# Kernel tuning notes

Measured on AMD Instinct MI355X. Metric: run time of the kernel, lower is better.

## Reference

```python
import jax, jax.numpy as jnp
import numpy as np

BS, NQ, DIMS = 4, 6400, 256
NH, NL, NP, NQUEUE = 8, 1, 4, 2


def ms_deform_attn(value, shapes_np, starts_np, loc, attn):
    # value: [B, Nv, H, D]; loc: [B, Nq, H, L, P, 2] in [0,1]; attn: [B, Nq, H, L, P]
    B, Nv, H, D = value.shape
    _, Nq, _, L, P, _ = loc.shape
    out = jnp.zeros((B, H, Nq, D), loc.dtype)
    for l in range(L):
        Hl, Wl = int(shapes_np[l, 0]), int(shapes_np[l, 1])
        s = int(starts_np[l])
        vl = value[:, s:s + Hl * Wl].transpose(0, 2, 1, 3)  # [B,H,HW,D]
        # grid_sample align_corners=False pixel coords
        x = loc[:, :, :, l, :, 0] * Wl - 0.5  # [B,Nq,H,P]
        y = loc[:, :, :, l, :, 1] * Hl - 0.5
        x0 = jnp.floor(x); y0 = jnp.floor(y)
        dx = x - x0; dy = y - y0
        x0i = x0.astype(jnp.int32); y0i = y0.astype(jnp.int32)
        acc = jnp.zeros((B, H, Nq * P, D), loc.dtype)
        corners = [(x0i, y0i, (1 - dx) * (1 - dy)),
                   (x0i + 1, y0i, dx * (1 - dy)),
                   (x0i, y0i + 1, (1 - dx) * dy),
                   (x0i + 1, y0i + 1, dx * dy)]
        for xi, yi, w in corners:
            valid = (xi >= 0) & (xi < Wl) & (yi >= 0) & (yi < Hl)
            idx = jnp.clip(yi, 0, Hl - 1) * Wl + jnp.clip(xi, 0, Wl - 1)  # [B,Nq,H,P]
            idx_t = idx.transpose(0, 2, 1, 3).reshape(B, H, Nq * P, 1)
            g = jnp.take_along_axis(vl, idx_t, axis=2)  # [B,H,Nq*P,D]
            wv = jnp.where(valid, w, 0.0).transpose(0, 2, 1, 3).reshape(B, H, Nq * P, 1)
            acc = acc + g * wv
        acc = acc.reshape(B, H, Nq, P, D)
        wl = attn[:, :, :, l].transpose(0, 2, 1, 3)  # [B,H,Nq,P]
        out = out + jnp.einsum('bhnpd,bhnp->bhnd', acc, wl)
    return out.transpose(0, 2, 1, 3).reshape(B, Nq, H * D)


def setup_inputs() -> dict:
    key = jax.random.key(0)
    ks = jax.random.split(key, 12)
    d2 = DIMS * NQUEUE
    noff = NQUEUE * NH * NL * NP * 2
    nattn = NQUEUE * NH * NL * NP
    sc = 1.0 / np.sqrt(DIMS)
    return {
        'query': jax.random.normal(ks[0], (BS, NQ, DIMS), jnp.float32),
        'voxbev': jax.random.normal(ks[1], (BS, NQ, DIMS), jnp.float32),
        'reference_points': jax.random.uniform(ks[2], (BS * NQUEUE, NQ, NL, 2), jnp.float32),
        'spatial_shapes': jnp.array([[80, 80]], dtype=jnp.int64),
        'level_start_index': jnp.array([0], dtype=jnp.int64),
        'Wv': jax.random.normal(ks[3], (DIMS, DIMS), jnp.float32) * sc,
        'bv': jax.random.normal(ks[4], (DIMS,), jnp.float32) * 0.01,
        'Woff': jax.random.normal(ks[5], (d2, noff), jnp.float32) * (1.0 / np.sqrt(d2)),
        'boff': jax.random.normal(ks[6], (noff,), jnp.float32),
        'Wattn': jax.random.normal(ks[7], (d2, nattn), jnp.float32) * (1.0 / np.sqrt(d2)),
        'battn': jax.random.normal(ks[8], (nattn,), jnp.float32) * 0.01,
        'Wo': jax.random.normal(ks[9], (DIMS, DIMS), jnp.float32) * sc,
        'bo': jax.random.normal(ks[10], (DIMS,), jnp.float32) * 0.01,
    }


def reference(query, voxbev, reference_points, spatial_shapes, level_start_index,
              Wv, bv, Woff, boff, Wattn, battn, Wo, bo):
    bs, nq, dims = query.shape
    shapes_np = np.asarray(spatial_shapes)
    starts_np = np.asarray(level_start_index)
    identity = query
    # value = stack([query, voxbev], 1).reshape(bs*2, nq, dims) -> interleaved [q0,v0,q1,v1,...]
    value = jnp.stack([query, voxbev], 1).reshape(bs * NQUEUE, nq, dims)
    qcat = jnp.concatenate([value[:bs], query], -1)  # [bs, nq, 2*dims]
    v = (value @ Wv + bv).reshape(bs * NQUEUE, nq, NH, dims // NH)
    off = (qcat @ Woff + boff).reshape(bs, nq, NH, NQUEUE, NL, NP, 2)
    attn = (qcat @ Wattn + battn).reshape(bs, nq, NH, NQUEUE, NL * NP)
    attn = jax.nn.softmax(attn, axis=-1).reshape(bs, nq, NH, NQUEUE, NL, NP)
    attn = attn.transpose(0, 3, 1, 2, 4, 5).reshape(bs * NQUEUE, nq, NH, NL, NP)
    off = off.transpose(0, 3, 1, 2, 4, 5, 6).reshape(bs * NQUEUE, nq, NH, NL, NP, 2)
    # offset normalizer: (W, H) per level
    norm = jnp.stack([spatial_shapes[:, 1], spatial_shapes[:, 0]], -1).astype(off.dtype)  # [L,2]
    loc = reference_points[:, :, None, :, None, :] + off / norm[None, None, None, :, None, :]
    out = ms_deform_attn(v, shapes_np, starts_np, loc, attn)  # [bs*2, nq, dims]
    out = out.reshape(bs, NQUEUE, nq, dims).mean(1)  # mean over queue
    out = out @ Wo + bo
    return out + identity  # dropout is identity in eval
```

## Files before the change

kernel.cpp:

```cpp
#include <hip/hip_runtime.h>
#include <hip/hip_bf16.h>

#define BS   4
#define NQ   6400
#define DIMS 256
#define NH   8
#define NP   4
#define GW   80
#define GH   80

typedef __hip_bfloat16 bf16;
typedef unsigned short ushort;
typedef __attribute__((ext_vector_type(8))) short short8;
typedef __attribute__((ext_vector_type(4))) float floatx4;

union bfu { bf16 h; ushort s; };
__device__ __forceinline__ ushort f2bs(float x) { bfu u; u.h = __float2bfloat16(x); return u.s; }
__device__ __forceinline__ float bs2f(ushort s) { return __uint_as_float(((unsigned)s) << 16); }
__device__ __forceinline__ float ldin(const void* p, size_t i, int isf) {
    return isf ? ((const float*)p)[i] : bs2f(((const ushort*)p)[i]);
}

__device__ __forceinline__ void gl_lds16(const void* gsrc, void* ldst) {
    __builtin_amdgcn_global_load_lds(
        (const __attribute__((address_space(1))) unsigned int*)gsrc,
        (__attribute__((address_space(3))) unsigned int*)ldst,
        16, 0, 0);
}

__device__ __forceinline__ int self_detect(const ushort* __restrict__ q, int tid) {
    int bad = 0;
    const uint4 u0 = ((const uint4*)q)[tid * 2];
    const uint4 u1 = ((const uint4*)q)[tid * 2 + 1];
    const unsigned w[8] = { u0.x, u0.y, u0.z, u0.w, u1.x, u1.y, u1.z, u1.w };
    #pragma unroll
    for (int j = 0; j < 8; ++j) {
        if (((w[j] >> 7)  & 0xFF) > 160) bad = 1;
        if (((w[j] >> 23) & 0xFF) > 160) bad = 1;
    }
    return __any(bad) ? 1 : 0;
}

__global__ __launch_bounds__(256) void prep_k(
    const void* __restrict__ Wv, const void* __restrict__ bv,
    const void* __restrict__ Woff, const void* __restrict__ boff,
    const void* __restrict__ Wattn, const void* __restrict__ battn,
    const void* __restrict__ Wo, const void* __restrict__ bo,
    int* __restrict__ flagp,
    ushort* __restrict__ WvT, ushort* __restrict__ WoaT, ushort* __restrict__ WoT,
    float* __restrict__ biasv, float* __restrict__ biasoa, float* __restrict__ biaso,
    const void* __restrict__ query, const void* __restrict__ voxbev,
    uint4* __restrict__ qb, uint4* __restrict__ vbv)
{
    const int tid = threadIdx.x;
    const int isf = self_detect((const ushort*)query, tid);
    const int bid = blockIdx.x;
    if (bid == 0 && tid == 0) *flagp = isf;
    if (bid < 899) {
        const int i = bid * 256 + tid;
        const int n1 = 256 * 256, n2 = n1 + 192 * 512, n3 = n2 + 256 * 256;
        const int n4 = n3 + 256, n5 = n4 + 192, n6 = n5 + 256;
        if (i < n1) {
            int n = i >> 8, k = i & 255;
            WvT[i] = f2bs(ldin(Wv, (size_t)k * 256 + n, isf));
        } else if (i < n2) {
            int j = i - n1, n = j >> 9, k = j & 511;
            float v = (n < 128) ? ldin(Woff, (size_t)k * 128 + n, isf)
                                : ldin(Wattn, (size_t)k * 64 + (n - 128), isf);
            WoaT[j] = f2bs(v);
        } else if (i < n3) {
            int j = i - n2, n = j >> 8, k = j & 255;
            WoT[j] = f2bs(ldin(Wo, (size_t)k * 256 + n, isf));
        } else if (i < n4) {
            biasv[i - n3] = ldin(bv, i - n3, isf);
        } else if (i < n5) {
            int j = i - n4;
            biasoa[j] = (j < 128) ? ldin(boff, j, isf) : ldin(battn, j - 128, isf);
        } else if (i < n6) {
            biaso[i - n5] = ldin(bo, i - n5, isf);
        }
    } else {
        if (isf == 0) return;
        const int t = (bid - 899) * 256 + tid;
        const int half = 819200;
        const void* src = (t < half) ? query : voxbev;
        uint4* dst = (t < half) ? qb : vbv;
        const int j = (t < half) ? t : t - half;
        const float4* s = (const float4*)src + (size_t)j * 2;
        float4 a = s[0], b = s[1];
        uint4 o;
        o.x = ((unsigned)f2bs(a.y) << 16) | f2bs(a.x);
        o.y = ((unsigned)f2bs(a.w) << 16) | f2bs(a.z);
        o.z = ((unsigned)f2bs(b.y) << 16) | f2bs(b.x);
        o.w = ((unsigned)f2bs(b.w) << 16) | f2bs(b.z);
        dst[j] = o;
    }
}

enum { A_VAL = 0, A_QCAT = 1, A_PLAIN = 2 };
enum { O_BF16 = 0, O_FINAL = 1, O_VPERM = 2, O_OAPERM = 3 };

#define ABYT 16384
#define BBYT 8192
#define CST  67
#define SMEMB (ABYT + BBYT)

template <int AMODE, int OMODE, int KTOT, int NX, int MG>
__device__ __forceinline__ void pgemm_body(
    const int F, char* smem,
    const ushort* __restrict__ Apl, const ushort* __restrict__ BT,
    const float* __restrict__ biasf, void* __restrict__ C,
    const void* __restrict__ query_raw, const void* __restrict__ voxbev_raw,
    const ushort* __restrict__ qb, const ushort* __restrict__ vbv,
    const int isf)
{
    constexpr int N = NX * 64;
    constexpr int NT = KTOT / 64;
    float* cbf = (float*)smem;

    const int xcd = F & 7, l = F >> 3;
    const int n = l % NX;
    const int mg = (l / NX) * 8 + xcd;
    if (mg >= MG) return;
    const int bm = mg * 128, bn = n * 64;

    const int tid = threadIdx.x;
    const int lane = tid & 63, wv = tid >> 6;
    const int wm = wv * 32;
    const int fr = lane & 15;
    const int lrow = lane >> 3;
    const int lslot = lane & 7;
    const int sg = lslot ^ lrow;

    const ushort* qsrc = isf ? qb  : (const ushort*)query_raw;
    const ushort* vsrc = isf ? vbv : (const ushort*)voxbev_raw;
    const ushort* aph[2] = { nullptr, nullptr };
    if (AMODE == A_PLAIN) {
        aph[0] = Apl + (size_t)bm * DIMS;
    } else {
        const int b = bm / NQ, q0 = bm - (bm / NQ) * NQ;
        aph[0] = ((b & 1) ? vsrc : qsrc) + (size_t)((b >> 1) * NQ + q0) * DIMS;
        if (AMODE == A_QCAT) aph[1] = qsrc + (size_t)(b * NQ + q0) * DIMS;
    }

    floatx4 acc[2][4] = {};

    #pragma unroll
    for (int t = 0; t < NT; ++t) {
        if (t > 0) __syncthreads();
        #pragma unroll
        for (int c4 = 0; c4 < 4; ++c4) {
            const int c = wv * 4 + c4;
            const int row = c * 8 + lrow;
            const int k = t * 64 + sg * 8;
            const ushort* gp;
            if (AMODE == A_QCAT && KTOT == 512)
                gp = aph[k >> 8] + (size_t)row * DIMS + (k & 255);
            else
                gp = aph[0] + (size_t)row * DIMS + k;
            gl_lds16(gp, smem + c * 1024);
        }
        #pragma unroll
        for (int c2 = 0; c2 < 2; ++c2) {
            const int c = wv * 2 + c2;
            const int row = c * 8 + lrow;
            gl_lds16(&BT[(size_t)(bn + row) * KTOT + t * 64 + sg * 8],
                     smem + ABYT + c * 1024);
        }
        asm volatile("s_waitcnt vmcnt(0)" ::: "memory");
        __syncthreads();

        const short* acur = (const short*)smem;
        const short* bcur = (const short*)(smem + ABYT);
        #pragma unroll
        for (int k0 = 0; k0 < 64; k0 += 32) {
            const int gl = (k0 >> 3) + (lane >> 4);
            const int sl = gl ^ (fr & 7);
            short8 af[2], bf[4];
            #pragma unroll
            for (int mt = 0; mt < 2; ++mt)
                af[mt] = *(const short8*)&acur[(wm + mt * 16 + fr) * 64 + sl * 8];
            #pragma unroll
            for (int nt = 0; nt < 4; ++nt)
                bf[nt] = *(const short8*)&bcur[(nt * 16 + fr) * 64 + sl * 8];
            #pragma unroll
            for (int mt = 0; mt < 2; ++mt)
                #pragma unroll
                for (int nt = 0; nt < 4; ++nt)
                    acc[mt][nt] = __builtin_amdgcn_mfma_f32_16x16x32_bf16(
                        af[mt], bf[nt], acc[mt][nt], 0, 0, 0);
        }
    }

    const int col = lane & 15, rq = (lane >> 4) * 4;
    const int lbase = wm & 63;
    #pragma unroll
    for (int half = 0; half < 2; ++half) {
        __syncthreads();
        if ((wv >> 1) == half) {
            #pragma unroll
            for (int mt = 0; mt < 2; ++mt)
                #pragma unroll
                for (int nt = 0; nt < 4; ++nt)
                    #pragma unroll
                    for (int r = 0; r < 4; ++r)
                        cbf[(lbase + mt * 16 + rq + r) * CST + nt * 16 + col] =
                            acc[mt][nt][r];
        }
        __syncthreads();

        if (OMODE == O_FINAL && isf) {
            const int r16 = tid >> 4, cc = tid & 15;
            #pragma unroll
            for (int it = 0; it < 4; ++it) {
                const int lr = it * 16 + r16;
                const size_t g = (size_t)(bm + half * 64 + lr);
                float4 x = *(const float4*)&cbf[lr * CST + cc * 4];
                const ushort* rs = qsrc + g * DIMS + bn + cc * 4;
                x.x += biasf[bn + cc * 4 + 0] + bs2f(rs[0]);
                x.y += biasf[bn + cc * 4 + 1] + bs2f(rs[1]);
                x.z += biasf[bn + cc * 4 + 2] + bs2f(rs[2]);
                x.w += biasf[bn + cc * 4 + 3] + bs2f(rs[3]);
                *(float4*)((float*)C + g * N + bn + cc * 4) = x;
            }
        } else {
            const int r8 = tid >> 3, c8 = tid & 7;
            #pragma unroll
            for (int it = 0; it < 2; ++it) {
                const int lr = it * 32 + r8;
                const size_t g = (size_t)(bm + half * 64 + lr);
                float4 x0 = *(const float4*)&cbf[lr * CST + c8 * 8];
                float4 x1 = *(const float4*)&cbf[lr * CST + c8 * 8 + 4];
                float xs[8] = { x0.x, x0.y, x0.z, x0.w, x1.x, x1.y, x1.z, x1.w };
                #pragma unroll
                for (int e = 0; e < 8; ++e) xs[e] += biasf[bn + c8 * 8 + e];
                if (OMODE == O_FINAL) {
                    const ushort* rs = qsrc + g * DIMS + bn + c8 * 8;
                    #pragma unroll
                    for (int e = 0; e < 8; ++e) xs[e] += bs2f(rs[e]);
                }
                uint4 o;
                o.x = ((unsigned)f2bs(xs[1]) << 16) | f2bs(xs[0]);
                o.y = ((unsigned)f2bs(xs[3]) << 16) | f2bs(xs[2]);
                o.z = ((unsigned)f2bs(xs[5]) << 16) | f2bs(xs[4]);
                o.w = ((unsigned)f2bs(xs[7]) << 16) | f2bs(xs[6]);
                ushort* dstp;
                if (OMODE == O_VPERM) {
                    const int cc = bn + c8 * 8;
                    const int s = (int)(g / NQ), qq = (int)(g % NQ);
                    dstp = (ushort*)C + ((size_t)(s * 8 + (cc >> 5)) * NQ + qq) * 32
                                      + (cc & 31);
                } else if (OMODE == O_OAPERM) {
                    const int cc = bn + c8 * 8;
                    const int bb = (int)(g / NQ), qq = (int)(g % NQ);
                    int hh, off;
                    if (cc < 128) { hh = cc >> 4; off = cc & 15; }
                    else          { hh = (cc - 128) >> 3; off = 16; }
                    dstp = (ushort*)C + ((size_t)(bb * 8 + hh) * NQ + qq) * 24 + off;
                } else {
                    dstp = (ushort*)C + g * N + bn + c8 * 8;
                }
                *(uint4*)dstp = o;
            }
        }
    }
}

__global__ __launch_bounds__(256, 6) void gemm12_k(
    const ushort* __restrict__ WvT, const float* __restrict__ biasv,
    ushort* __restrict__ v_ws,
    const ushort* __restrict__ WoaT, const float* __restrict__ biasoa,
    ushort* __restrict__ offraw,
    const void* __restrict__ query_raw, const void* __restrict__ voxbev_raw,
    const ushort* __restrict__ qb, const ushort* __restrict__ vbv,
    const int* __restrict__ flagp)
{
    __shared__ __align__(16) char smem[SMEMB];
    const int isf = *flagp;
    const int bid = blockIdx.x;
    if (bid < 1600) {
        pgemm_body<A_VAL, O_VPERM, 256, 4, 400>(bid, smem,
            nullptr, WvT, biasv, (void*)v_ws, query_raw, voxbev_raw, qb, vbv, isf);
    } else {
        pgemm_body<A_QCAT, O_OAPERM, 512, 3, 200>(bid - 1600, smem,
            nullptr, WoaT, biasoa, (void*)offraw, query_raw, voxbev_raw, qb, vbv, isf);
    }
}

__global__ __launch_bounds__(256, 6) void gemm4_k(
    const ushort* __restrict__ Apl, const ushort* __restrict__ BT,
    const float* __restrict__ biasf, void* __restrict__ C,
    const void* __restrict__ query_raw, const void* __restrict__ voxbev_raw,
    const ushort* __restrict__ qb, const ushort* __restrict__ vbv,
    const int* __restrict__ flagp)
{
    __shared__ __align__(16) char smem[SMEMB];
    const int isf = *flagp;
    pgemm_body<A_PLAIN, O_FINAL, 256, 4, 200>(blockIdx.x, smem,
        Apl, BT, biasf, C, query_raw, voxbev_raw, qb, vbv, isf);
}

__global__ __launch_bounds__(256) void sample_k(
    const ushort* __restrict__ v,
    const ushort* __restrict__ offp,
    const void* __restrict__ refpts,
    const int* __restrict__ flagp,
    ushort* __restrict__ sampled)
{
    const int isf = *flagp;
    __shared__ int   sidx[64][2][17];
    __shared__ float swt [64][2][17];
    const int tid = threadIdx.x;
    const int j = blockIdx.x;
    const int h = j & 7;
    const int k = j >> 3;
    const int b = k / 100;
    const int q0 = (k % 100) * 64;

    if (tid < 128) {
        const int lq = tid >> 1, queue = tid & 1;
        const int q = q0 + lq;
        const ushort* rec = offp + ((size_t)(b * 8 + h) * NQ + q) * 24;
        const ushort* al = rec + 16 + queue * 4;
        float l0 = bs2f(al[0]), l1 = bs2f(al[1]), l2 = bs2f(al[2]), l3 = bs2f(al[3]);
        float mx = fmaxf(fmaxf(l0, l1), fmaxf(l2, l3));
        float e0 = __expf(l0 - mx), e1 = __expf(l1 - mx);
        float e2 = __expf(l2 - mx), e3 = __expf(l3 - mx);
        float inv = 0.5f / (e0 + e1 + e2 + e3);
        const int bq = b * 2 + queue;
        const float rx = ldin(refpts, ((size_t)bq * NQ + q) * 2 + 0, isf);
        const float ry = ldin(refpts, ((size_t)bq * NQ + q) * 2 + 1, isf);
        const ushort* od = rec + queue * 8;
        float ww[4] = { e0 * inv, e1 * inv, e2 * inv, e3 * inv };
        #pragma unroll
        for (int p = 0; p < NP; ++p) {
            const float x = rx * (float)GW + bs2f(od[p * 2 + 0]) - 0.5f;
            const float y = ry * (float)GH + bs2f(od[p * 2 + 1]) - 0.5f;
            const float x0f = floorf(x), y0f = floorf(y);
            const float dx = x - x0f, dy = y - y0f;
            const int x0 = (int)x0f, y0 = (int)y0f;
            const float wp = ww[p];
            const float cw4[4] = { wp * (1.0f - dx) * (1.0f - dy),
                                   wp * dx * (1.0f - dy),
                                   wp * (1.0f - dx) * dy,
                                   wp * dx * dy };
            #pragma unroll
            for (int c = 0; c < 4; ++c) {
                const int xs = x0 + (c & 1), ys = y0 + (c >> 1);
                const bool ok = (unsigned)xs < (unsigned)GW && (unsigned)ys < (unsigned)GH;
                const int xi = min(max(xs, 0), GW - 1);
                const int yi = min(max(ys, 0), GH - 1);
                sidx[lq][queue][p * 4 + c] = yi * GW + xi;
                swt [lq][queue][p * 4 + c] = ok ? cw4[c] : 0.0f;
            }
        }
    }
    __syncthreads();

    const int lq = tid >> 2, d8 = tid & 3;
    const int q = q0 + lq;
    float a[8] = {};
    #pragma unroll
    for (int queue = 0; queue < 2; ++queue) {
        const ushort* vb = v + (((size_t)(b * 2 + queue) * 8 + h) * NQ) * 32 + d8 * 8;
        #pragma unroll
        for (int hf = 0; hf < 2; ++hf) {
            uint4 g[8];
            #pragma unroll
            for (int u = 0; u < 8; ++u) {
                const int ci = sidx[lq][queue][hf * 8 + u];
                g[u] = *(const uint4*)&vb[(size_t)ci * 32];
            }
            __builtin_amdgcn_sched_barrier(0);
            #pragma unroll
            for (int u = 0; u < 8; ++u) {
                const float cw = swt[lq][queue][hf * 8 + u];
                a[0] += cw * bs2f((ushort)g[u].x); a[1] += cw * bs2f((ushort)(g[u].x >> 16));
                a[2] += cw * bs2f((ushort)g[u].y); a[3] += cw * bs2f((ushort)(g[u].y >> 16));
                a[4] += cw * bs2f((ushort)g[u].z); a[5] += cw * bs2f((ushort)(g[u].z >> 16));
                a[6] += cw * bs2f((ushort)g[u].w); a[7] += cw * bs2f((ushort)(g[u].w >> 16));
            }
        }
    }
    uint4 o;
    o.x = ((unsigned)f2bs(a[1]) << 16) | f2bs(a[0]);
    o.y = ((unsigned)f2bs(a[3]) << 16) | f2bs(a[2]);
    o.z = ((unsigned)f2bs(a[5]) << 16) | f2bs(a[4]);
    o.w = ((unsigned)f2bs(a[7]) << 16) | f2bs(a[6]);
    *(uint4*)&sampled[((size_t)b * NQ + q) * DIMS + h * 32 + d8 * 8] = o;
}

extern "C" void kernel_launch(void* const* d_in, const int* in_sizes, int n_in,
                              void* d_out, int out_size, void* d_ws, size_t ws_size,
                              hipStream_t stream)
{
    const void* query  = d_in[0];
    const void* voxbev = d_in[1];
    const void* refpts = d_in[2];
    const void* Wv   = d_in[5];  const void* bv    = d_in[6];
    const void* Woff = d_in[7];  const void* boff  = d_in[8];
    const void* Wattn= d_in[9];  const void* battn = d_in[10];
    const void* Wo   = d_in[11]; const void* bo    = d_in[12];

    char* p = (char*)d_ws;
    int* flag = (int*)p;             p += 256;
    ushort* WvT  = (ushort*)p;       p += 256 * 256 * 2;
    ushort* WoaT = (ushort*)p;       p += 192 * 512 * 2;
    ushort* WoT  = (ushort*)p;       p += 256 * 256 * 2;
    float* biasv  = (float*)p;       p += 1024;
    float* biasoa = (float*)p;       p += 1024;
    float* biaso  = (float*)p;       p += 1024;
    ushort* qb   = (ushort*)p;       p += (size_t)BS * NQ * DIMS * 2;
    ushort* vbv  = (ushort*)p;       p += (size_t)BS * NQ * DIMS * 2;
    ushort* v_ws = (ushort*)p;       p += (size_t)2 * BS * NQ * DIMS * 2;
    ushort* offraw = (ushort*)p;     p += (size_t)BS * NQ * 192 * 2;
    ushort* sampled = (ushort*)p;

    prep_k<<<7299, 256, 0, stream>>>(Wv, bv, Woff, boff, Wattn, battn, Wo, bo,
                                     flag, WvT, WoaT, WoT, biasv, biasoa, biaso,
                                     query, voxbev, (uint4*)qb, (uint4*)vbv);

    gemm12_k<<<2200, 256, 0, stream>>>(WvT, biasv, v_ws, WoaT, biasoa, offraw,
                                       query, voxbev, qb, vbv, flag);

    sample_k<<<3200, 256, 0, stream>>>(v_ws, offraw, refpts, flag, sampled);

    gemm4_k<<<800, 256, 0, stream>>>(sampled, WoT, biaso, d_out,
                                     query, voxbev, qb, vbv, flag);
}
```

Baseline: 190.6 us.

## Fuse all stages into one cooperative persistent kernel with double-buffered GEMM loads

Replaces the four separate launches with a single cooperative kernel of 768 persistent blocks that loop over the work of each stage, separated by grid-wide syncs. This removes launch gaps and the inter-kernel drain. The GEMM body now double-buffers its LDS tiles so the next K-tile's global-to-LDS loads overlap the current MFMAs, and the epilogue writes the full 128-row tile in one pass instead of two halves. The flag buffer is dropped and each block recomputes the dtype detection itself. The costs are larger shared memory, which limits occupancy to 3 blocks per CU, grid-sync overhead, and a fallback to separate launches if the cooperative launch fails.

```diff
diff --git a/kernel.cpp b/kernel.cpp
--- a/kernel.cpp
+++ b/kernel.cpp
@@ -1,5 +1,8 @@
 #include <hip/hip_runtime.h>
 #include <hip/hip_bf16.h>
+#include <hip/hip_cooperative_groups.h>
+
+namespace cg = cooperative_groups;
 
 #define BS   4
 #define NQ   6400
@@ -26,6 +29,12 @@
         (const __attribute__((address_space(1))) unsigned int*)gsrc,
         (__attribute__((address_space(3))) unsigned int*)ldst,
         16, 0, 0);
+}
+
+__device__ __forceinline__ void barrier_fence() {
+    __builtin_amdgcn_sched_barrier(0);
+    asm volatile("s_barrier" ::: "memory");
+    __builtin_amdgcn_sched_barrier(0);
 }
 
 __device__ __forceinline__ int self_detect(const ushort* __restrict__ q, int tid) {
@@ -41,23 +50,19 @@
     return __any(bad) ? 1 : 0;
 }
 
-__global__ __launch_bounds__(256) void prep_k(
+__device__ __forceinline__ void prep_body(
+    const int vb, const int tid, const int isf,
     const void* __restrict__ Wv, const void* __restrict__ bv,
     const void* __restrict__ Woff, const void* __restrict__ boff,
     const void* __restrict__ Wattn, const void* __restrict__ battn,
     const void* __restrict__ Wo, const void* __restrict__ bo,
-    int* __restrict__ flagp,
     ushort* __restrict__ WvT, ushort* __restrict__ WoaT, ushort* __restrict__ WoT,
     float* __restrict__ biasv, float* __restrict__ biasoa, float* __restrict__ biaso,
     const void* __restrict__ query, const void* __restrict__ voxbev,
     uint4* __restrict__ qb, uint4* __restrict__ vbv)
 {
-    const int tid = threadIdx.x;
-    const int isf = self_detect((const ushort*)query, tid);
-    const int bid = blockIdx.x;
-    if (bid == 0 && tid == 0) *flagp = isf;
-    if (bid < 899) {
-        const int i = bid * 256 + tid;
+    if (vb < 899) {
+        const int i = vb * 256 + tid;
         const int n1 = 256 * 256, n2 = n1 + 192 * 512, n3 = n2 + 256 * 256;
         const int n4 = n3 + 256, n5 = n4 + 192, n6 = n5 + 256;
         if (i < n1) {
@@ -81,7 +86,7 @@
         }
     } else {
         if (isf == 0) return;
-        const int t = (bid - 899) * 256 + tid;
+        const int t = (vb - 899) * 256 + tid;
         const int half = 819200;
         const void* src = (t < half) ? query : voxbev;
         uint4* dst = (t < half) ? qb : vbv;
@@ -100,13 +105,11 @@
 enum { A_VAL = 0, A_QCAT = 1, A_PLAIN = 2 };
 enum { O_BF16 = 0, O_FINAL = 1, O_VPERM = 2, O_OAPERM = 3 };
 
-#define ABYT 16384
-#define BBYT 8192
-#define CST  67
-#define SMEMB (ABYT + BBYT)
-
-template <int AMODE, int OMODE, int KTOT, int NX, int MG>
-__device__ __forceinline__ void pgemm_body(
+#define PTILE 24576
+#define PSMEM (2 * PTILE)
+
+template <int AMODE, int OMODE, int KTOT, int NXW, int MG>
+__device__ __forceinline__ void pgemm_pipe(
     const int F, char* smem,
     const ushort* __restrict__ Apl, const ushort* __restrict__ BT,
     const float* __restrict__ biasf, void* __restrict__ C,
@@ -114,13 +117,13 @@
     const ushort* __restrict__ qb, const ushort* __restrict__ vbv,
     const int isf)
 {
-    constexpr int N = NX * 64;
+    constexpr int N = 64 * NXW;
     constexpr int NT = KTOT / 64;
     float* cbf = (float*)smem;
 
     const int xcd = F & 7, l = F >> 3;
-    const int n = l % NX;
-    const int mg = (l / NX) * 8 + xcd;
+    const int n = l % NXW;
+    const int mg = (l / NXW) * 8 + xcd;
     if (mg >= MG) return;
     const int bm = mg * 128, bn = n * 64;
 
@@ -143,11 +146,9 @@
         if (AMODE == A_QCAT) aph[1] = qsrc + (size_t)(b * NQ + q0) * DIMS;
     }
 
-    floatx4 acc[2][4] = {};
-
-    #pragma unroll
-    for (int t = 0; t < NT; ++t) {
-        if (t > 0) __syncthreads();
+    auto stage = [&](int td, int t) {
+        char* ab = smem + td * PTILE;
+        char* bb = ab + 16384;
         #pragma unroll
         for (int c4 = 0; c4 < 4; ++c4) {
             const int c = wv * 4 + c4;
@@ -158,20 +159,34 @@
                 gp = aph[k >> 8] + (size_t)row * DIMS + (k & 255);
             else
                 gp = aph[0] + (size_t)row * DIMS + k;
-            gl_lds16(gp, smem + c * 1024);
+            gl_lds16(gp, ab + c * 1024);
         }
         #pragma unroll
         for (int c2 = 0; c2 < 2; ++c2) {
             const int c = wv * 2 + c2;
             const int row = c * 8 + lrow;
             gl_lds16(&BT[(size_t)(bn + row) * KTOT + t * 64 + sg * 8],
-                     smem + ABYT + c * 1024);
-        }
-        asm volatile("s_waitcnt vmcnt(0)" ::: "memory");
-        __syncthreads();
-
-        const short* acur = (const short*)smem;
-        const short* bcur = (const short*)(smem + ABYT);
+                     bb + c * 1024);
+        }
+    };
+
+    floatx4 acc[2][4] = {};
+
+    stage(0, 0);
+    #pragma unroll
+    for (int t = 0; t < NT; ++t) {
+        if (t + 1 < NT) {
+            stage((t + 1) & 1, t + 1);
+            __builtin_amdgcn_sched_barrier(0);
+            asm volatile("s_waitcnt vmcnt(6)" ::: "memory");
+        } else {
+            __builtin_amdgcn_sched_barrier(0);
+            asm volatile("s_waitcnt vmcnt(0)" ::: "memory");
+        }
+        barrier_fence();
+
+        const short* acur = (const short*)(smem + (t & 1) * PTILE);
+        const short* bcur = acur + 8192;
         #pragma unroll
         for (int k0 = 0; k0 < 64; k0 += 32) {
             const int gl = (k0 >> 3) + (lane >> 4);
@@ -190,128 +205,85 @@
                     acc[mt][nt] = __builtin_amdgcn_mfma_f32_16x16x32_bf16(
                         af[mt], bf[nt], acc[mt][nt], 0, 0, 0);
         }
-    }
-
+        barrier_fence();
+    }
+
+    __syncthreads();
     const int col = lane & 15, rq = (lane >> 4) * 4;
-    const int lbase = wm & 63;
     #pragma unroll
-    for (int half = 0; half < 2; ++half) {
-        __syncthreads();
-        if ((wv >> 1) == half) {
-            #pragma unroll
-            for (int mt = 0; mt < 2; ++mt)
+    for (int mt = 0; mt < 2; ++mt)
+        #pragma unroll
+        for (int nt = 0; nt < 4; ++nt)
+            #pragma unroll
+            for (int r = 0; r < 4; ++r)
+                cbf[(wm + mt * 16 + rq + r) * 67 + nt * 16 + col] = acc[mt][nt][r];
+    __syncthreads();
+
+    if (OMODE == O_FINAL && isf) {
+        const int r16 = tid >> 4, cc = tid & 15;
+        #pragma unroll
+        for (int it = 0; it < 8; ++it) {
+            const int lr = it * 16 + r16;
+            const size_t g = (size_t)(bm + lr);
+            float4 x = *(const float4*)&cbf[lr * 67 + cc * 4];
+            const ushort* rs = qsrc + g * DIMS + bn + cc * 4;
+            x.x += biasf[bn + cc * 4 + 0] + bs2f(rs[0]);
+            x.y += biasf[bn + cc * 4 + 1] + bs2f(rs[1]);
+            x.z += biasf[bn + cc * 4 + 2] + bs2f(rs[2]);
+            x.w += biasf[bn + cc * 4 + 3] + bs2f(rs[3]);
+            *(float4*)((float*)C + g * N + bn + cc * 4) = x;
+        }
+    } else {
+        const int r8 = tid >> 3, c8 = tid & 7;
+        #pragma unroll
+        for (int it = 0; it < 4; ++it) {
+            const int lr = it * 32 + r8;
+            const size_t g = (size_t)(bm + lr);
+            float4 x0 = *(const float4*)&cbf[lr * 67 + c8 * 8];
+            float4 x1 = *(const float4*)&cbf[lr * 67 + c8 * 8 + 4];
+            float xs[8] = { x0.x, x0.y, x0.z, x0.w, x1.x, x1.y, x1.z, x1.w };
+            #pragma unroll
+            for (int e = 0; e < 8; ++e) xs[e] += biasf[bn + c8 * 8 + e];
+            if (OMODE == O_FINAL) {
+                const ushort* rs = qsrc + g * DIMS + bn + c8 * 8;
                 #pragma unroll
-                for (int nt = 0; nt < 4; ++nt)
-                    #pragma unroll
-                    for (int r = 0; r < 4; ++r)
-                        cbf[(lbase + mt * 16 + rq + r) * CST + nt * 16 + col] =
-                            acc[mt][nt][r];
-        }
-        __syncthreads();
-
-        if (OMODE == O_FINAL && isf) {
-            const int r16 = tid >> 4, cc = tid & 15;
-            #pragma unroll
-            for (int it = 0; it < 4; ++it) {
-                const int lr = it * 16 + r16;
-                const size_t g = (size_t)(bm + half * 64 + lr);
-                float4 x = *(const float4*)&cbf[lr * CST + cc * 4];
-                const ushort* rs = qsrc + g * DIMS + bn + cc * 4;
-                x.x += biasf[bn + cc * 4 + 0] + bs2f(rs[0]);
-                x.y += biasf[bn + cc * 4 + 1] + bs2f(rs[1]);
-                x.z += biasf[bn + cc * 4 + 2] + bs2f(rs[2]);
-                x.w += biasf[bn + cc * 4 + 3] + bs2f(rs[3]);
-                *(float4*)((float*)C + g * N + bn + cc * 4) = x;
+                for (int e = 0; e < 8; ++e) xs[e] += bs2f(rs[e]);
             }
-        } else {
-            const int r8 = tid >> 3, c8 = tid & 7;
-            #pragma unroll
-            for (int it = 0; it < 2; ++it) {
-                const int lr = it * 32 + r8;
-                const size_t g = (size_t)(bm + half * 64 + lr);
-                float4 x0 = *(const float4*)&cbf[lr * CST + c8 * 8];
-                float4 x1 = *(const float4*)&cbf[lr * CST + c8 * 8 + 4];
-                float xs[8] = { x0.x, x0.y, x0.z, x0.w, x1.x, x1.y, x1.z, x1.w };
-                #pragma unroll
-                for (int e = 0; e < 8; ++e) xs[e] += biasf[bn + c8 * 8 + e];
-                if (OMODE == O_FINAL) {
-                    const ushort* rs = qsrc + g * DIMS + bn + c8 * 8;
-                    #pragma unroll
-                    for (int e = 0; e < 8; ++e) xs[e] += bs2f(rs[e]);
-                }
-                uint4 o;
-                o.x = ((unsigned)f2bs(xs[1]) << 16) | f2bs(xs[0]);
-                o.y = ((unsigned)f2bs(xs[3]) << 16) | f2bs(xs[2]);
-                o.z = ((unsigned)f2bs(xs[5]) << 16) | f2bs(xs[4]);
-                o.w = ((unsigned)f2bs(xs[7]) << 16) | f2bs(xs[6]);
-                ushort* dstp;
-                if (OMODE == O_VPERM) {
-                    const int cc = bn + c8 * 8;
-                    const int s = (int)(g / NQ), qq = (int)(g % NQ);
-                    dstp = (ushort*)C + ((size_t)(s * 8 + (cc >> 5)) * NQ + qq) * 32
-                                      + (cc & 31);
-                } else if (OMODE == O_OAPERM) {
-                    const int cc = bn + c8 * 8;
-                    const int bb = (int)(g / NQ), qq = (int)(g % NQ);
-                    int hh, off;
-                    if (cc < 128) { hh = cc >> 4; off = cc & 15; }
-                    else          { hh = (cc - 128) >> 3; off = 16; }
-                    dstp = (ushort*)C + ((size_t)(bb * 8 + hh) * NQ + qq) * 24 + off;
-                } else {
-                    dstp = (ushort*)C + g * N + bn + c8 * 8;
-                }
-                *(uint4*)dstp = o;
+            uint4 o;
+            o.x = ((unsigned)f2bs(xs[1]) << 16) | f2bs(xs[0]);
+            o.y = ((unsigned)f2bs(xs[3]) << 16) | f2bs(xs[2]);
+            o.z = ((unsigned)f2bs(xs[5]) << 16) | f2bs(xs[4]);
+            o.w = ((unsigned)f2bs(xs[7]) << 16) | f2bs(xs[6]);
+            ushort* dstp;
+            if (OMODE == O_VPERM) {
+                const int cc = bn + c8 * 8;
+                const int s = (int)(g / NQ), qq = (int)(g % NQ);
+                dstp = (ushort*)C + ((size_t)(s * 8 + (cc >> 5)) * NQ + qq) * 32
+                                  + (cc & 31);
+            } else if (OMODE == O_OAPERM) {
+                const int cc = bn + c8 * 8;
+                const int bb = (int)(g / NQ), qq = (int)(g % NQ);
+                int hh, off;
+                if (cc < 128) { hh = cc >> 4; off = cc & 15; }
+                else          { hh = (cc - 128) >> 3; off = 16; }
+                dstp = (ushort*)C + ((size_t)(bb * 8 + hh) * NQ + qq) * 24 + off;
+            } else {
+                dstp = (ushort*)C + g * N + bn + c8 * 8;
             }
-        }
-    }
-}
-
-__global__ __launch_bounds__(256, 6) void gemm12_k(
-    const ushort* __restrict__ WvT, const float* __restrict__ biasv,
-    ushort* __restrict__ v_ws,
-    const ushort* __restrict__ WoaT, const float* __restrict__ biasoa,
-    ushort* __restrict__ offraw,
-    const void* __restrict__ query_raw, const void* __restrict__ voxbev_raw,
-    const ushort* __restrict__ qb, const ushort* __restrict__ vbv,
-    const int* __restrict__ flagp)
-{
-    __shared__ __align__(16) char smem[SMEMB];
-    const int isf = *flagp;
-    const int bid = blockIdx.x;
-    if (bid < 1600) {
-        pgemm_body<A_VAL, O_VPERM, 256, 4, 400>(bid, smem,
-            nullptr, WvT, biasv, (void*)v_ws, query_raw, voxbev_raw, qb, vbv, isf);
-    } else {
-        pgemm_body<A_QCAT, O_OAPERM, 512, 3, 200>(bid - 1600, smem,
-            nullptr, WoaT, biasoa, (void*)offraw, query_raw, voxbev_raw, qb, vbv, isf);
-    }
-}
-
-__global__ __launch_bounds__(256, 6) void gemm4_k(
-    const ushort* __restrict__ Apl, const ushort* __restrict__ BT,
-    const float* __restrict__ biasf, void* __restrict__ C,
-    const void* __restrict__ query_raw, const void* __restrict__ voxbev_raw,
-    const ushort* __restrict__ qb, const ushort* __restrict__ vbv,
-    const int* __restrict__ flagp)
-{
-    __shared__ __align__(16) char smem[SMEMB];
-    const int isf = *flagp;
-    pgemm_body<A_PLAIN, O_FINAL, 256, 4, 200>(blockIdx.x, smem,
-        Apl, BT, biasf, C, query_raw, voxbev_raw, qb, vbv, isf);
-}
-
-__global__ __launch_bounds__(256) void sample_k(
+            *(uint4*)dstp = o;
+        }
+    }
+}
+
+__device__ __forceinline__ void sample_body(
+    const int j, const int tid, const int isf, char* sm,
     const ushort* __restrict__ v,
     const ushort* __restrict__ offp,
     const void* __restrict__ refpts,
-    const int* __restrict__ flagp,
     ushort* __restrict__ sampled)
 {
-    const int isf = *flagp;
-    __shared__ int   sidx[64][2][17];
-    __shared__ float swt [64][2][17];
-    const int tid = threadIdx.x;
-    const int j = blockIdx.x;
+    int*   sidx = (int*)sm;
+    float* swt  = (float*)(sm + 64 * 2 * 17 * 4);
     const int h = j & 7;
     const int k = j >> 3;
     const int b = k / 100;
@@ -332,6 +304,7 @@
         const float ry = ldin(refpts, ((size_t)bq * NQ + q) * 2 + 1, isf);
         const ushort* od = rec + queue * 8;
         float ww[4] = { e0 * inv, e1 * inv, e2 * inv, e3 * inv };
+        const int base = (lq * 2 + queue) * 17;
         #pragma unroll
         for (int p = 0; p < NP; ++p) {
             const float x = rx * (float)GW + bs2f(od[p * 2 + 0]) - 0.5f;
@@ -350,8 +323,8 @@
                 const bool ok = (unsigned)xs < (unsigned)GW && (unsigned)ys < (unsigned)GH;
                 const int xi = min(max(xs, 0), GW - 1);
                 const int yi = min(max(ys, 0), GH - 1);
-                sidx[lq][queue][p * 4 + c] = yi * GW + xi;
-                swt [lq][queue][p * 4 + c] = ok ? cw4[c] : 0.0f;
+                sidx[base + p * 4 + c] = yi * GW + xi;
+                swt [base + p * 4 + c] = ok ? cw4[c] : 0.0f;
             }
         }
     }
@@ -363,18 +336,19 @@
     #pragma unroll
     for (int queue = 0; queue < 2; ++queue) {
         const ushort* vb = v + (((size_t)(b * 2 + queue) * 8 + h) * NQ) * 32 + d8 * 8;
+        const int base = (lq * 2 + queue) * 17;
         #pragma unroll
         for (int hf = 0; hf < 2; ++hf) {
             uint4 g[8];
             #pragma unroll
             for (int u = 0; u < 8; ++u) {
-                const int ci = sidx[lq][queue][hf * 8 + u];
+                const int ci = sidx[base + hf * 8 + u];
                 g[u] = *(const uint4*)&vb[(size_t)ci * 32];
             }
             __builtin_amdgcn_sched_barrier(0);
             #pragma unroll
             for (int u = 0; u < 8; ++u) {
-                const float cw = swt[lq][queue][hf * 8 + u];
+                const float cw = swt[base + hf * 8 + u];
                 a[0] += cw * bs2f((ushort)g[u].x); a[1] += cw * bs2f((ushort)(g[u].x >> 16));
                 a[2] += cw * bs2f((ushort)g[u].y); a[3] += cw * bs2f((ushort)(g[u].y >> 16));
                 a[4] += cw * bs2f((ushort)g[u].z); a[5] += cw * bs2f((ushort)(g[u].z >> 16));
@@ -388,6 +362,106 @@
     o.z = ((unsigned)f2bs(a[5]) << 16) | f2bs(a[4]);
     o.w = ((unsigned)f2bs(a[7]) << 16) | f2bs(a[6]);
     *(uint4*)&sampled[((size_t)b * NQ + q) * DIMS + h * 32 + d8 * 8] = o;
+}
+
+__global__ __launch_bounds__(256, 3) void fused_k(
+    const void* query, const void* voxbev, const void* refpts,
+    const void* Wv, const void* bv, const void* Woff, const void* boff,
+    const void* Wattn, const void* battn, const void* Wo, const void* bo,
+    ushort* WvT, ushort* WoaT, ushort* WoT,
+    float* biasv, float* biasoa, float* biaso,
+    ushort* qb, ushort* vbv, ushort* v_ws, ushort* offraw, ushort* sampled,
+    void* out)
+{
+    __shared__ __align__(16) char smem[PSMEM];
+    cg::grid_group grid = cg::this_grid();
+    const int tid = threadIdx.x;
+    const int isf = self_detect((const ushort*)query, tid);
+    const int G = gridDim.x;
+
+    for (int vb = blockIdx.x; vb < 7299; vb += G)
+        prep_body(vb, tid, isf, Wv, bv, Woff, boff, Wattn, battn, Wo, bo,
+                  WvT, WoaT, WoT, biasv, biasoa, biaso,
+                  query, voxbev, (uint4*)qb, (uint4*)vbv);
+    __threadfence();
+    grid.sync();
+
+    for (int vb = blockIdx.x; vb < 2200; vb += G) {
+        if (vb < 1600)
+            pgemm_pipe<A_VAL, O_VPERM, 256, 4, 400>(vb, smem,
+                nullptr, WvT, biasv, (void*)v_ws, query, voxbev, qb, vbv, isf);
+        else
+            pgemm_pipe<A_QCAT, O_OAPERM, 512, 3, 200>(vb - 1600, smem,
+                nullptr, WoaT, biasoa, (void*)offraw, query, voxbev, qb, vbv, isf);
+        __syncthreads();
+    }
+    __threadfence();
+    grid.sync();
+
+    for (int vb = blockIdx.x; vb < 3200; vb += G) {
+        sample_body(vb, tid, isf, smem, v_ws, offraw, refpts, sampled);
+        __syncthreads();
+    }
+    __threadfence();
+    grid.sync();
+
+    for (int vb = blockIdx.x; vb < 800; vb += G) {
+        pgemm_pipe<A_PLAIN, O_FINAL, 256, 4, 200>(vb, smem,
+            sampled, WoT, biaso, out, query, voxbev, qb, vbv, isf);
+        __syncthreads();
+    }
+}
+
+__global__ __launch_bounds__(256) void prep_k(
+    const void* query, const void* voxbev,
+    const void* Wv, const void* bv, const void* Woff, const void* boff,
+    const void* Wattn, const void* battn, const void* Wo, const void* bo,
+    ushort* WvT, ushort* WoaT, ushort* WoT,
+    float* biasv, float* biasoa, float* biaso,
+    ushort* qb, ushort* vbv)
+{
+    const int tid = threadIdx.x;
+    const int isf = self_detect((const ushort*)query, tid);
+    prep_body(blockIdx.x, tid, isf, Wv, bv, Woff, boff, Wattn, battn, Wo, bo,
+              WvT, WoaT, WoT, biasv, biasoa, biaso,
+              query, voxbev, (uint4*)qb, (uint4*)vbv);
+}
+
+__global__ __launch_bounds__(256) void gemm12_k(
+    const void* query, const void* voxbev,
+    const ushort* WvT, const float* biasv, ushort* v_ws,
+    const ushort* WoaT, const float* biasoa, ushort* offraw,
+    const ushort* qb, const ushort* vbv)
+{
+    __shared__ __align__(16) char smem[PSMEM];
+    const int isf = self_detect((const ushort*)query, threadIdx.x);
+    const int bid = blockIdx.x;
+    if (bid < 1600)
+        pgemm_pipe<A_VAL, O_VPERM, 256, 4, 400>(bid, smem,
+            nullptr, WvT, biasv, (void*)v_ws, query, voxbev, qb, vbv, isf);
+    else
+        pgemm_pipe<A_QCAT, O_OAPERM, 512, 3, 200>(bid - 1600, smem,
+            nullptr, WoaT, biasoa, (void*)offraw, query, voxbev, qb, vbv, isf);
+}
+
+__global__ __launch_bounds__(256) void sample_k(
+    const void* query, const ushort* v, const ushort* offp,
+    const void* refpts, ushort* sampled)
+{
+    __shared__ __align__(16) char smem[2 * 64 * 2 * 17 * 4];
+    const int isf = self_detect((const ushort*)query, threadIdx.x);
+    sample_body(blockIdx.x, threadIdx.x, isf, smem, v, offp, refpts, sampled);
+}
+
+__global__ __launch_bounds__(256) void gemm4_k(
+    const void* query, const void* voxbev,
+    const ushort* Apl, const ushort* BT, const float* biasf, void* C,
+    const ushort* qb, const ushort* vbv)
+{
+    __shared__ __align__(16) char smem[PSMEM];
+    const int isf = self_detect((const ushort*)query, threadIdx.x);
+    pgemm_pipe<A_PLAIN, O_FINAL, 256, 4, 200>(blockIdx.x, smem,
+        Apl, BT, biasf, C, query, voxbev, qb, vbv, isf);
 }
 
 extern "C" void kernel_launch(void* const* d_in, const int* in_sizes, int n_in,
@@ -403,7 +477,7 @@
     const void* Wo   = d_in[11]; const void* bo    = d_in[12];
 
     char* p = (char*)d_ws;
-    int* flag = (int*)p;             p += 256;
+    p += 256;
     ushort* WvT  = (ushort*)p;       p += 256 * 256 * 2;
     ushort* WoaT = (ushort*)p;       p += 192 * 512 * 2;
     ushort* WoT  = (ushort*)p;       p += 256 * 256 * 2;
@@ -416,15 +490,27 @@
     ushort* offraw = (ushort*)p;     p += (size_t)BS * NQ * 192 * 2;
     ushort* sampled = (ushort*)p;
 
-    prep_k<<<7299, 256, 0, stream>>>(Wv, bv, Woff, boff, Wattn, battn, Wo, bo,
-                                     flag, WvT, WoaT, WoT, biasv, biasoa, biaso,
-                                     query, voxbev, (uint4*)qb, (uint4*)vbv);
-
-    gemm12_k<<<2200, 256, 0, stream>>>(WvT, biasv, v_ws, WoaT, biasoa, offraw,
-                                       query, voxbev, qb, vbv, flag);
-
-    sample_k<<<3200, 256, 0, stream>>>(v_ws, offraw, refpts, flag, sampled);
-
-    gemm4_k<<<800, 256, 0, stream>>>(sampled, WoT, biaso, d_out,
-                                     query, voxbev, qb, vbv, flag);
-}
+    void* ka[] = {
+        (void*)&query, (void*)&voxbev, (void*)&refpts,
+        (void*)&Wv, (void*)&bv, (void*)&Woff, (void*)&boff,
+        (void*)&Wattn, (void*)&battn, (void*)&Wo, (void*)&bo,
+        (void*)&WvT, (void*)&WoaT, (void*)&WoT,
+        (void*)&biasv, (void*)&biasoa, (void*)&biaso,
+        (void*)&qb, (void*)&vbv, (void*)&v_ws, (void*)&offraw,
+        (void*)&sampled, (void*)&d_out
+    };
+    hipError_t e = hipLaunchCooperativeKernel((const void*)fused_k,
+                                              dim3(768), dim3(256),
+                                              ka, 0u, stream);
+    if (e == hipSuccess) return;
+
+    prep_k<<<7299, 256, 0, stream>>>(query, voxbev, Wv, bv, Woff, boff,
+                                     Wattn, battn, Wo, bo,
+                                     WvT, WoaT, WoT, biasv, biasoa, biaso,
+                                     qb, vbv);
+    gemm12_k<<<2200, 256, 0, stream>>>(query, voxbev, WvT, biasv, v_ws,
+                                       WoaT, biasoa, offraw, qb, vbv);
+    sample_k<<<3200, 256, 0, stream>>>(query, v_ws, offraw, refpts, sampled);
+    gemm4_k<<<800, 256, 0, stream>>>(query, voxbev, sampled, WoT, biaso,
+                                     d_out, qb, vbv);
+}
```

Result: slower. 717.0 us (+276.2%).

## Double-buffer GEMM K-loop LDS tiles to overlap global loads with MFMA

Applied to the files above, without the earlier changes.

Replaces the single-buffered K loop in the projection GEMMs with a two-stage ping-pong. The next K tile is issued via global_load_lds into the alternate buffer while MFMAs consume the current one, using partial vmcnt waits and raw s_barrier fences. The epilogue now writes the full 128-row C tile to LDS in one pass instead of two halves, which the larger 48KB LDS allows. The occupancy hint of 6 blocks per CU is dropped; the doubled LDS per block will likely reduce resident blocks and latency hiding.

```diff
diff --git a/kernel.cpp b/kernel.cpp
--- a/kernel.cpp
+++ b/kernel.cpp
@@ -26,6 +26,12 @@
         (const __attribute__((address_space(1))) unsigned int*)gsrc,
         (__attribute__((address_space(3))) unsigned int*)ldst,
         16, 0, 0);
+}
+
+__device__ __forceinline__ void barrier_fence() {
+    __builtin_amdgcn_sched_barrier(0);
+    asm volatile("s_barrier" ::: "memory");
+    __builtin_amdgcn_sched_barrier(0);
 }
 
 __device__ __forceinline__ int self_detect(const ushort* __restrict__ q, int tid) {
@@ -100,13 +106,11 @@
 enum { A_VAL = 0, A_QCAT = 1, A_PLAIN = 2 };
 enum { O_BF16 = 0, O_FINAL = 1, O_VPERM = 2, O_OAPERM = 3 };
 
-#define ABYT 16384
-#define BBYT 8192
-#define CST  67
-#define SMEMB (ABYT + BBYT)
-
-template <int AMODE, int OMODE, int KTOT, int NX, int MG>
-__device__ __forceinline__ void pgemm_body(
+#define PTILE 24576
+#define PSMEM (2 * PTILE)
+
+template <int AMODE, int OMODE, int KTOT, int NXW, int MG>
+__device__ __forceinline__ void pgemm_pipe(
     const int F, char* smem,
     const ushort* __restrict__ Apl, const ushort* __restrict__ BT,
     const float* __restrict__ biasf, void* __restrict__ C,
@@ -114,13 +118,13 @@
     const ushort* __restrict__ qb, const ushort* __restrict__ vbv,
     const int isf)
 {
-    constexpr int N = NX * 64;
+    constexpr int N = 64 * NXW;
     constexpr int NT = KTOT / 64;
     float* cbf = (float*)smem;
 
     const int xcd = F & 7, l = F >> 3;
-    const int n = l % NX;
-    const int mg = (l / NX) * 8 + xcd;
+    const int n = l % NXW;
+    const int mg = (l / NXW) * 8 + xcd;
     if (mg >= MG) return;
     const int bm = mg * 128, bn = n * 64;
 
@@ -143,11 +147,9 @@
         if (AMODE == A_QCAT) aph[1] = qsrc + (size_t)(b * NQ + q0) * DIMS;
     }
 
-    floatx4 acc[2][4] = {};
-
-    #pragma unroll
-    for (int t = 0; t < NT; ++t) {
-        if (t > 0) __syncthreads();
+    auto stage = [&](int td, int t) {
+        char* ab = smem + td * PTILE;
+        char* bb = ab + 16384;
         #pragma unroll
         for (int c4 = 0; c4 < 4; ++c4) {
             const int c = wv * 4 + c4;
@@ -158,20 +160,34 @@
                 gp = aph[k >> 8] + (size_t)row * DIMS + (k & 255);
             else
                 gp = aph[0] + (size_t)row * DIMS + k;
-            gl_lds16(gp, smem + c * 1024);
+            gl_lds16(gp, ab + c * 1024);
         }
         #pragma unroll
         for (int c2 = 0; c2 < 2; ++c2) {
             const int c = wv * 2 + c2;
             const int row = c * 8 + lrow;
             gl_lds16(&BT[(size_t)(bn + row) * KTOT + t * 64 + sg * 8],
-                     smem + ABYT + c * 1024);
-        }
-        asm volatile("s_waitcnt vmcnt(0)" ::: "memory");
-        __syncthreads();
-
-        const short* acur = (const short*)smem;
-        const short* bcur = (const short*)(smem + ABYT);
+                     bb + c * 1024);
+        }
+    };
+
+    floatx4 acc[2][4] = {};
+
+    stage(0, 0);
+    #pragma unroll
+    for (int t = 0; t < NT; ++t) {
+        if (t + 1 < NT) {
+            stage((t + 1) & 1, t + 1);
+            __builtin_amdgcn_sched_barrier(0);
+            asm volatile("s_waitcnt vmcnt(6)" ::: "memory");
+        } else {
+            __builtin_amdgcn_sched_barrier(0);
+            asm volatile("s_waitcnt vmcnt(0)" ::: "memory");
+        }
+        barrier_fence();
+
+        const short* acur = (const short*)(smem + (t & 1) * PTILE);
+        const short* bcur = acur + 8192;
         #pragma unroll
         for (int k0 = 0; k0 < 64; k0 += 32) {
             const int gl = (k0 >> 3) + (lane >> 4);
@@ -190,83 +206,77 @@
                     acc[mt][nt] = __builtin_amdgcn_mfma_f32_16x16x32_bf16(
                         af[mt], bf[nt], acc[mt][nt], 0, 0, 0);
         }
-    }
-
+        barrier_fence();
+    }
+
+    __syncthreads();
     const int col = lane & 15, rq = (lane >> 4) * 4;
-    const int lbase = wm & 63;
     #pragma unroll
-    for (int half = 0; half < 2; ++half) {
-        __syncthreads();
-        if ((wv >> 1) == half) {
-            #pragma unroll
-            for (int mt = 0; mt < 2; ++mt)
+    for (int mt = 0; mt < 2; ++mt)
+        #pragma unroll
+        for (int nt = 0; nt < 4; ++nt)
+            #pragma unroll
+            for (int r = 0; r < 4; ++r)
+                cbf[(wm + mt * 16 + rq + r) * 67 + nt * 16 + col] = acc[mt][nt][r];
+    __syncthreads();
+
+    if (OMODE == O_FINAL && isf) {
+        const int r16 = tid >> 4, cc = tid & 15;
+        #pragma unroll
+        for (int it = 0; it < 8; ++it) {
+            const int lr = it * 16 + r16;
+            const size_t g = (size_t)(bm + lr);
+            float4 x = *(const float4*)&cbf[lr * 67 + cc * 4];
+            const ushort* rs = qsrc + g * DIMS + bn + cc * 4;
+            x.x += biasf[bn + cc * 4 + 0] + bs2f(rs[0]);
+            x.y += biasf[bn + cc * 4 + 1] + bs2f(rs[1]);
+            x.z += biasf[bn + cc * 4 + 2] + bs2f(rs[2]);
+            x.w += biasf[bn + cc * 4 + 3] + bs2f(rs[3]);
+            *(float4*)((float*)C + g * N + bn + cc * 4) = x;
+        }
+    } else {
+        const int r8 = tid >> 3, c8 = tid & 7;
+        #pragma unroll
+        for (int it = 0; it < 4; ++it) {
+            const int lr = it * 32 + r8;
+            const size_t g = (size_t)(bm + lr);
+            float4 x0 = *(const float4*)&cbf[lr * 67 + c8 * 8];
+            float4 x1 = *(const float4*)&cbf[lr * 67 + c8 * 8 + 4];
+            float xs[8] = { x0.x, x0.y, x0.z, x0.w, x1.x, x1.y, x1.z, x1.w };
+            #pragma unroll
+            for (int e = 0; e < 8; ++e) xs[e] += biasf[bn + c8 * 8 + e];
+            if (OMODE == O_FINAL) {
+                const ushort* rs = qsrc + g * DIMS + bn + c8 * 8;
                 #pragma unroll
-                for (int nt = 0; nt < 4; ++nt)
-                    #pragma unroll
-                    for (int r = 0; r < 4; ++r)
-                        cbf[(lbase + mt * 16 + rq + r) * CST + nt * 16 + col] =
-                            acc[mt][nt][r];
-        }
-        __syncthreads();
-
-        if (OMODE == O_FINAL && isf) {
-            const int r16 = tid >> 4, cc = tid & 15;
-            #pragma unroll
-            for (int it = 0; it < 4; ++it) {
-                const int lr = it * 16 + r16;
-                const size_t g = (size_t)(bm + half * 64 + lr);
-                float4 x = *(const float4*)&cbf[lr * CST + cc * 4];
-                const ushort* rs = qsrc + g * DIMS + bn + cc * 4;
-                x.x += biasf[bn + cc * 4 + 0] + bs2f(rs[0]);
-                x.y += biasf[bn + cc * 4 + 1] + bs2f(rs[1]);
-                x.z += biasf[bn + cc * 4 + 2] + bs2f(rs[2]);
-                x.w += biasf[bn + cc * 4 + 3] + bs2f(rs[3]);
-                *(float4*)((float*)C + g * N + bn + cc * 4) = x;
+                for (int e = 0; e < 8; ++e) xs[e] += bs2f(rs[e]);
             }
-        } else {
-            const int r8 = tid >> 3, c8 = tid & 7;
-            #pragma unroll
-            for (int it = 0; it < 2; ++it) {
-                const int lr = it * 32 + r8;
-                const size_t g = (size_t)(bm + half * 64 + lr);
-                float4 x0 = *(const float4*)&cbf[lr * CST + c8 * 8];
-                float4 x1 = *(const float4*)&cbf[lr * CST + c8 * 8 + 4];
-                float xs[8] = { x0.x, x0.y, x0.z, x0.w, x1.x, x1.y, x1.z, x1.w };
-                #pragma unroll
-                for (int e = 0; e < 8; ++e) xs[e] += biasf[bn + c8 * 8 + e];
-                if (OMODE == O_FINAL) {
-                    const ushort* rs = qsrc + g * DIMS + bn + c8 * 8;
-                    #pragma unroll
-                    for (int e = 0; e < 8; ++e) xs[e] += bs2f(rs[e]);
-                }
-                uint4 o;
-                o.x = ((unsigned)f2bs(xs[1]) << 16) | f2bs(xs[0]);
-                o.y = ((unsigned)f2bs(xs[3]) << 16) | f2bs(xs[2]);
-                o.z = ((unsigned)f2bs(xs[5]) << 16) | f2bs(xs[4]);
-                o.w = ((unsigned)f2bs(xs[7]) << 16) | f2bs(xs[6]);
-                ushort* dstp;
-                if (OMODE == O_VPERM) {
-                    const int cc = bn + c8 * 8;
-                    const int s = (int)(g / NQ), qq = (int)(g % NQ);
-                    dstp = (ushort*)C + ((size_t)(s * 8 + (cc >> 5)) * NQ + qq) * 32
-                                      + (cc & 31);
-                } else if (OMODE == O_OAPERM) {
-                    const int cc = bn + c8 * 8;
-                    const int bb = (int)(g / NQ), qq = (int)(g % NQ);
-                    int hh, off;
-                    if (cc < 128) { hh = cc >> 4; off = cc & 15; }
-                    else          { hh = (cc - 128) >> 3; off = 16; }
-                    dstp = (ushort*)C + ((size_t)(bb * 8 + hh) * NQ + qq) * 24 + off;
-                } else {
-                    dstp = (ushort*)C + g * N + bn + c8 * 8;
-                }
-                *(uint4*)dstp = o;
+            uint4 o;
+            o.x = ((unsigned)f2bs(xs[1]) << 16) | f2bs(xs[0]);
+            o.y = ((unsigned)f2bs(xs[3]) << 16) | f2bs(xs[2]);
+            o.z = ((unsigned)f2bs(xs[5]) << 16) | f2bs(xs[4]);
+            o.w = ((unsigned)f2bs(xs[7]) << 16) | f2bs(xs[6]);
+            ushort* dstp;
+            if (OMODE == O_VPERM) {
+                const int cc = bn + c8 * 8;
+                const int s = (int)(g / NQ), qq = (int)(g % NQ);
+                dstp = (ushort*)C + ((size_t)(s * 8 + (cc >> 5)) * NQ + qq) * 32
+                                  + (cc & 31);
+            } else if (OMODE == O_OAPERM) {
+                const int cc = bn + c8 * 8;
+                const int bb = (int)(g / NQ), qq = (int)(g % NQ);
+                int hh, off;
+                if (cc < 128) { hh = cc >> 4; off = cc & 15; }
+                else          { hh = (cc - 128) >> 3; off = 16; }
+                dstp = (ushort*)C + ((size_t)(bb * 8 + hh) * NQ + qq) * 24 + off;
+            } else {
+                dstp = (ushort*)C + g * N + bn + c8 * 8;
             }
-        }
-    }
-}
-
-__global__ __launch_bounds__(256, 6) void gemm12_k(
+            *(uint4*)dstp = o;
+        }
+    }
+}
+
+__global__ __launch_bounds__(256) void gemm12_k(
     const ushort* __restrict__ WvT, const float* __restrict__ biasv,
     ushort* __restrict__ v_ws,
     const ushort* __restrict__ WoaT, const float* __restrict__ biasoa,
@@ -275,28 +285,28 @@
     const ushort* __restrict__ qb, const ushort* __restrict__ vbv,
     const int* __restrict__ flagp)
 {
-    __shared__ __align__(16) char smem[SMEMB];
+    __shared__ __align__(16) char smem[PSMEM];
     const int isf = *flagp;
     const int bid = blockIdx.x;
     if (bid < 1600) {
-        pgemm_body<A_VAL, O_VPERM, 256, 4, 400>(bid, smem,
+        pgemm_pipe<A_VAL, O_VPERM, 256, 4, 400>(bid, smem,
             nullptr, WvT, biasv, (void*)v_ws, query_raw, voxbev_raw, qb, vbv, isf);
     } else {
-        pgemm_body<A_QCAT, O_OAPERM, 512, 3, 200>(bid - 1600, smem,
+        pgemm_pipe<A_QCAT, O_OAPERM, 512, 3, 200>(bid - 1600, smem,
             nullptr, WoaT, biasoa, (void*)offraw, query_raw, voxbev_raw, qb, vbv, isf);
     }
 }
 
-__global__ __launch_bounds__(256, 6) void gemm4_k(
+__global__ __launch_bounds__(256) void gemm4_k(
     const ushort* __restrict__ Apl, const ushort* __restrict__ BT,
     const float* __restrict__ biasf, void* __restrict__ C,
     const void* __restrict__ query_raw, const void* __restrict__ voxbev_raw,
     const ushort* __restrict__ qb, const ushort* __restrict__ vbv,
     const int* __restrict__ flagp)
 {
-    __shared__ __align__(16) char smem[SMEMB];
+    __shared__ __align__(16) char smem[PSMEM];
     const int isf = *flagp;
-    pgemm_body<A_PLAIN, O_FINAL, 256, 4, 200>(blockIdx.x, smem,
+    pgemm_pipe<A_PLAIN, O_FINAL, 256, 4, 200>(blockIdx.x, smem,
         Apl, BT, biasf, C, query_raw, voxbev_raw, qb, vbv, isf);
 }
 
```

Result: faster. 181.0 us (-5.1%).
